# Optimization experiments

Measured on AMD Instinct MI355X. Metric: run time of the kernel, lower is better.

Reference implementation:

```python
import jax, jax.numpy as jnp
import numpy as np

KW = 3          # kernel_width
PAD = (KW - 1) // 2


def setup_inputs() -> dict:
    key = jax.random.key(0)
    ks = jax.random.split(key, 7)
    B, Lq, Lk, D, C = 8, 1024, 1024, 512, 512  # D=q_size, C=k_size
    return {
        "q": jax.random.normal(ks[0], (B, Lq, D), jnp.float32),
        "k": jax.random.normal(ks[1], (B, Lk, C), jnp.float32),
        "W_kernel": jax.random.normal(ks[2], (D, C * KW), jnp.float32) * (1.0 / np.sqrt(D)),
        "b_kernel": jax.random.normal(ks[3], (C * KW,), jnp.float32) * 0.02,
        "W_bias": jax.random.normal(ks[4], (D, 1), jnp.float32) * (1.0 / np.sqrt(D)),
        "b_bias": jax.random.normal(ks[5], (1,), jnp.float32) * 0.02,
        "bias_b": jax.random.normal(ks[6], (1,), jnp.float32),
    }


def reference(q, k, W_kernel, b_kernel, W_bias, b_bias, bias_b):
    B, Lq, D = q.shape
    _, Lk, C = k.shape
    # per-(batch, query) dynamic conv kernels: [B, Lq, C, KW]
    kernel = (q @ W_kernel + b_kernel).reshape(B, Lq, C, KW)
    # per-(batch, query) scalar bias: [B, Lq]
    bias = (q @ W_bias + b_bias)[..., 0]
    # windowed view of k (cross-correlation with 'same' padding)
    kpad = jnp.pad(k, ((0, 0), (PAD, PAD), (0, 0)))  # [B, Lk+2*PAD, C]
    win_idx = jnp.arange(Lk)[:, None] + jnp.arange(KW)[None, :]  # [Lk, KW]
    kwin = kpad[:, win_idx, :]  # [B, Lk, KW, C]
    # a[b,i,j] = sum_{c,w} kernel[b,i,c,w] * kpad[b, j+w, c] + bias[b,i] + bias_b
    a_ij = jnp.einsum('bicw,bjwc->bij', kernel, kwin)
    return a_ij + bias[:, :, None] + bias_b
```

## Files before the change

kernel.cpp:

```cpp
#include <hip/hip_runtime.h>


typedef __attribute__((ext_vector_type(8))) short s8vec;
typedef __attribute__((ext_vector_type(4))) float floatx4;

__device__ __forceinline__ unsigned short f2bf(float f) {
    union { float f; unsigned u; } v; v.f = f;
    unsigned r = (v.u + 0x7FFFu + ((v.u >> 16) & 1u)) >> 16;
    return (unsigned short)r;
}

__device__ __forceinline__ float bf2f(unsigned short s) {
    union { unsigned u; float f; } v; v.u = ((unsigned)s) << 16;
    return v.f;
}

__device__ __forceinline__ void gl2lds16(const void* g, void* l) {
    __builtin_amdgcn_global_load_lds(
        (__attribute__((address_space(1))) void*)(g),
        (__attribute__((address_space(3))) void*)(l), 16, 0, 0);
}

__global__ void cvt_all(const float* __restrict__ q, const float* __restrict__ k,
                        unsigned short* __restrict__ qbf, unsigned short* __restrict__ kp,
                        const float* __restrict__ W, unsigned short* __restrict__ Wt2,
                        const float* __restrict__ b_kernel) {
    int blk = blockIdx.x;
    if (blk < 4104) {
        int t = blk * 256 + threadIdx.x;
        if (t < 524288) {
            const float4* p = (const float4*)q + 2 * (size_t)t;
            float4 a = p[0], b = p[1];
            union { unsigned short s[8]; uint4 v; } o;
            o.s[0]=f2bf(a.x); o.s[1]=f2bf(a.y); o.s[2]=f2bf(a.z); o.s[3]=f2bf(a.w);
            o.s[4]=f2bf(b.x); o.s[5]=f2bf(b.y); o.s[6]=f2bf(b.z); o.s[7]=f2bf(b.w);
            ((uint4*)qbf)[t] = o.v;
        } else if (t < 1048576) {
            int e8 = t - 524288;
            size_t e = (size_t)e8 * 8;
            int b = e8 >> 16;
            int j = (e8 >> 6) & 1023;
            int c = (e8 & 63) * 8;
            const float4* p = (const float4*)(k + e);
            float4 a = p[0], bb = p[1];
            union { unsigned short s[8]; uint4 v; } o;
            o.s[0]=f2bf(a.x); o.s[1]=f2bf(a.y); o.s[2]=f2bf(a.z); o.s[3]=f2bf(a.w);
            o.s[4]=f2bf(bb.x); o.s[5]=f2bf(bb.y); o.s[6]=f2bf(bb.z); o.s[7]=f2bf(bb.w);
            *(uint4*)(kp + ((size_t)(b * 1028 + j + 1) * 512 + c)) = o.v;
        } else if (t < 1050624) {
            int z = t - 1048576;
            int b = z >> 8, r = (z >> 6) & 3, ch = z & 63;
            int row = r ? (1024 + r) : 0;
            *(uint4*)(kp + ((size_t)(b * 1028 + row) * 512 + ch * 8)) = make_uint4(0u,0u,0u,0u);
        }
    } else if (blk < 4616) {
        __shared__ float ldsw[1536];
        int d = blk - 4104;
        const float4* wrow = (const float4*)(W + (size_t)d * 1536);
        for (int e = threadIdx.x; e < 384; e += 256) {
            float4 v = wrow[e];
            float va[4] = { v.x, v.y, v.z, v.w };
            #pragma unroll
            for (int i = 0; i < 4; i++) {
                int idx = e * 4 + i;
                int c = idx / 3, w = idx - c * 3;
                ldsw[w * 512 + c] = va[i];
            }
        }
        __syncthreads();
        for (int p = threadIdx.x; p < 192; p += 256) {
            union { unsigned short s[8]; uint4 v; } o;
            #pragma unroll
            for (int i = 0; i < 8; i++) o.s[i] = f2bf(ldsw[p * 8 + i]);
            *(uint4*)(Wt2 + (size_t)d * 1536 + p * 8) = o.v;
        }
    } else {
        int u = (blk - 4616) * 256 + threadIdx.x;
        int row = 512 + u / 192;
        int p = u - (u / 192) * 192;
        union { unsigned short s[8]; uint4 v; } o;
        if (row == 512) {
            #pragma unroll
            for (int i = 0; i < 8; i++) {
                int lin = p * 8 + i;
                int w = lin >> 9, c = lin & 511;
                o.s[i] = f2bf(b_kernel[c * 3 + w]);
            }
        } else {
            o.v = make_uint4(0u, 0u, 0u, 0u);
        }
        *(uint4*)(Wt2 + (size_t)row * 1536 + p * 8) = o.v;
    }
}

__global__ __launch_bounds__(256) void gemm_V(const unsigned short* __restrict__ kp,
                                              const unsigned short* __restrict__ Wt2,
                                              const float* __restrict__ Wbias,
                                              unsigned short* __restrict__ V) {
    __shared__ unsigned short lds_a[2][128 * 32];
    __shared__ unsigned short lds_b[2][64 * 32];
    int g = blockIdx.x;
    int b = g & 7, slot = g >> 3;
    int j0 = (slot / 9) * 128;
    int n0 = (slot % 9) * 64;
    int tid = threadIdx.x, wid = tid >> 6, lane = tid & 63;
    int wm = wid >> 1, wn = wid & 1;
    int arow = lane >> 2, acol = (lane & 3) * 8;
    const unsigned short* kpb = kp + (size_t)(b * 1028 + j0) * 512;
    floatx4 acc[4][2] = {};

    auto STAGE = [&](int buf, int kk) {
        #pragma unroll
        for (int s = 0; s < 3; ++s) {
            int t = wid * 3 + s;
            if (t < 8) {
                const unsigned short* ga = kpb + (size_t)(t * 16 + arow) * 512 + kk + acol;
                gl2lds16(ga, (char*)lds_a[buf] + t * 1024);
            } else {
                int u = t - 8;
                const unsigned short* gb = Wt2 + (size_t)(n0 + u * 16 + arow) * 1536 + kk + acol;
                gl2lds16(gb, (char*)lds_b[buf] + u * 1024);
            }
        }
    };

    STAGE(0, 0);
    __syncthreads();
    int cur = 0;
    int ra = lane & 15, q8 = (lane >> 4) * 8;
    for (int kt = 0; kt < 48; ++kt) {
        if (kt < 47) STAGE(cur ^ 1, (kt + 1) * 32);
        s8vec af[4], bfr[2];
        #pragma unroll
        for (int mi = 0; mi < 4; mi++)
            af[mi] = *(const s8vec*)(&lds_a[cur][(wm * 64 + mi * 16 + ra) * 32 + q8]);
        #pragma unroll
        for (int ni = 0; ni < 2; ni++)
            bfr[ni] = *(const s8vec*)(&lds_b[cur][(wn * 32 + ni * 16 + ra) * 32 + q8]);
        #pragma unroll
        for (int mi = 0; mi < 4; mi++)
            #pragma unroll
            for (int ni = 0; ni < 2; ni++)
                acc[mi][ni] = __builtin_amdgcn_mfma_f32_16x16x32_bf16(af[mi], bfr[ni], acc[mi][ni], 0, 0, 0);
        if (kt < 47) { __syncthreads(); cur ^= 1; }
    }

    int cl = lane & 15, qd = lane >> 4;
    #pragma unroll
    for (int mi = 0; mi < 4; mi++) {
        #pragma unroll
        for (int ni = 0; ni < 2; ni++) {
            int col = n0 + wn * 32 + ni * 16 + cl;
            float wb = (col < 512) ? Wbias[col] : 0.0f;
            #pragma unroll
            for (int r = 0; r < 4; r++) {
                int m_g = b * 1024 + j0 + wm * 64 + mi * 16 + qd * 4 + r;
                V[(size_t)m_g * 576 + col] = f2bf(acc[mi][ni][r] + wb);
            }
        }
    }
}

__global__ __launch_bounds__(256) void gemm_QV(const unsigned short* __restrict__ qbf,
                                               const unsigned short* __restrict__ V,
                                               const float* __restrict__ b_bias,
                                               const float* __restrict__ bias_b,
                                               float* __restrict__ out) {
    __shared__ unsigned short lds_a[2][128 * 32];
    __shared__ unsigned short lds_b[2][128 * 32];
    int g = blockIdx.x;
    int b = g & 7, slot = g >> 3;
    int i0 = (slot >> 3) * 128;
    int j0 = (slot & 7) * 128;
    int tid = threadIdx.x, wid = tid >> 6, lane = tid & 63;
    int wm = wid >> 1, wn = wid & 1;
    int arow = lane >> 2, acol = (lane & 3) * 8;
    const unsigned short* Ab = qbf + (size_t)b * 1024 * 512;
    const unsigned short* Bb = V + (size_t)b * 1024 * 576;
    floatx4 acc[4][4] = {};

    auto STAGE = [&](int buf, int kk) {
        #pragma unroll
        for (int s = 0; s < 2; ++s) {
            int t = wid * 2 + s;
            const unsigned short* ga = Ab + (size_t)(i0 + t * 16 + arow) * 512 + kk + acol;
            gl2lds16(ga, (char*)lds_a[buf] + t * 1024);
            const unsigned short* gb = Bb + (size_t)(j0 + t * 16 + arow) * 576 + kk + acol;
            gl2lds16(gb, (char*)lds_b[buf] + t * 1024);
        }
    };

    STAGE(0, 0);
    __syncthreads();
    int cur = 0;
    int ra = lane & 15, q8 = (lane >> 4) * 8;
    for (int kt = 0; kt < 16; ++kt) {
        if (kt < 15) STAGE(cur ^ 1, (kt + 1) * 32);
        s8vec af[4], bfr[4];
        #pragma unroll
        for (int mi = 0; mi < 4; mi++)
            af[mi] = *(const s8vec*)(&lds_a[cur][(wm * 64 + mi * 16 + ra) * 32 + q8]);
        #pragma unroll
        for (int ni = 0; ni < 4; ni++)
            bfr[ni] = *(const s8vec*)(&lds_b[cur][(wn * 64 + ni * 16 + ra) * 32 + q8]);
        #pragma unroll
        for (int mi = 0; mi < 4; mi++)
            #pragma unroll
            for (int ni = 0; ni < 4; ni++)
                acc[mi][ni] = __builtin_amdgcn_mfma_f32_16x16x32_bf16(af[mi], bfr[ni], acc[mi][ni], 0, 0, 0);
        if (kt < 15) { __syncthreads(); cur ^= 1; }
    }

    int cl = lane & 15, qd = lane >> 4;
    float bbsum = b_bias[0] + bias_b[0];
    float tv[4];
    #pragma unroll
    for (int ni = 0; ni < 4; ni++) {
        int j_loc = wn * 64 + ni * 16 + cl;
        tv[ni] = bf2f(V[((size_t)(b * 1024 + j0 + j_loc)) * 576 + 512]) + bbsum;
    }
    #pragma unroll
    for (int mi = 0; mi < 4; mi++) {
        #pragma unroll
        for (int r = 0; r < 4; r++) {
            int i_g = i0 + wm * 64 + mi * 16 + qd * 4 + r;
            float* orow = out + ((size_t)(b * 1024 + i_g)) * 1024 + j0;
            #pragma unroll
            for (int ni = 0; ni < 4; ni++) {
                int j_loc = wn * 64 + ni * 16 + cl;
                orow[j_loc] = acc[mi][ni][r] + tv[ni];
            }
        }
    }
}

extern "C" void kernel_launch(void* const* d_in, const int* in_sizes, int n_in,
                              void* d_out, int out_size, void* d_ws, size_t ws_size,
                              hipStream_t stream) {
    const float* q        = (const float*)d_in[0];
    const float* k        = (const float*)d_in[1];
    const float* W_kernel = (const float*)d_in[2];
    const float* b_kernel = (const float*)d_in[3];
    const float* W_bias   = (const float*)d_in[4];
    const float* b_bias   = (const float*)d_in[5];
    const float* bias_b   = (const float*)d_in[6];
    float* out = (float*)d_out;

    char* ws = (char*)d_ws;
    unsigned short* q_bf = (unsigned short*)(ws);
    unsigned short* kp   = (unsigned short*)(ws + 8388608);
    unsigned short* Wt2  = (unsigned short*)(ws + 8388608 + 8421376 + 16384);
    unsigned short* V    = (unsigned short*)(ws + 8388608 + 8421376 + 16384 + 1769472);

    cvt_all<<<4664, 256, 0, stream>>>(q, k, q_bf, kp, W_kernel, Wt2, b_kernel);
    gemm_V<<<576, 256, 0, stream>>>(kp, Wt2, W_bias, V);
    gemm_QV<<<512, 256, 0, stream>>>(q_bf, V, b_bias, bias_b, out);
}
```

Measured before the change: 138.3 us.

## Compute b_kernel bias term separately, shrink V width, use K=64 tiles with XOR swizzle

Moves the b_kernel·kwin bias term out of the augmented GEMM into a separate fp32 reduction in the conversion kernel, so V becomes 512 wide instead of 576 and gemm_V needs 512 blocks instead of 576. Both GEMMs now stage 64-wide K tiles with an XOR-swizzled LDS layout, which halves the number of barriers and is meant to reduce LDS bank conflicts. The cost is double the LDS per block, which may lower occupancy, plus an extra 256-block reduction pass over k.

```diff
diff --git a/kernel.cpp b/kernel.cpp
--- a/kernel.cpp
+++ b/kernel.cpp
@@ -10,11 +10,6 @@
     return (unsigned short)r;
 }
 
-__device__ __forceinline__ float bf2f(unsigned short s) {
-    union { unsigned u; float f; } v; v.u = ((unsigned)s) << 16;
-    return v.f;
-}
-
 __device__ __forceinline__ void gl2lds16(const void* g, void* l) {
     __builtin_amdgcn_global_load_lds(
         (__attribute__((address_space(1))) void*)(g),
@@ -24,7 +19,8 @@
 __global__ void cvt_all(const float* __restrict__ q, const float* __restrict__ k,
                         unsigned short* __restrict__ qbf, unsigned short* __restrict__ kp,
                         const float* __restrict__ W, unsigned short* __restrict__ Wt2,
-                        const float* __restrict__ b_kernel) {
+                        const float* __restrict__ b_kernel, float* __restrict__ tj) {
+    __shared__ float ldsw[1536];
     int blk = blockIdx.x;
     if (blk < 4104) {
         int t = blk * 256 + threadIdx.x;
@@ -54,7 +50,6 @@
             *(uint4*)(kp + ((size_t)(b * 1028 + row) * 512 + ch * 8)) = make_uint4(0u,0u,0u,0u);
         }
     } else if (blk < 4616) {
-        __shared__ float ldsw[1536];
         int d = blk - 4104;
         const float4* wrow = (const float4*)(W + (size_t)d * 1536);
         for (int e = threadIdx.x; e < 384; e += 256) {
@@ -75,21 +70,39 @@
             *(uint4*)(Wt2 + (size_t)d * 1536 + p * 8) = o.v;
         }
     } else {
-        int u = (blk - 4616) * 256 + threadIdx.x;
-        int row = 512 + u / 192;
-        int p = u - (u / 192) * 192;
-        union { unsigned short s[8]; uint4 v; } o;
-        if (row == 512) {
-            #pragma unroll
-            for (int i = 0; i < 8; i++) {
-                int lin = p * 8 + i;
-                int w = lin >> 9, c = lin & 511;
-                o.s[i] = f2bf(b_kernel[c * 3 + w]);
-            }
-        } else {
-            o.v = make_uint4(0u, 0u, 0u, 0u);
-        }
-        *(uint4*)(Wt2 + (size_t)row * 1536 + p * 8) = o.v;
+        int p = blk - 4616;
+        int b = p >> 5, j0r = (p & 31) * 32;
+        for (int e = threadIdx.x; e < 1536; e += 256) {
+            float v = b_kernel[e];
+            int c = e / 3, w = e - c * 3;
+            ldsw[w * 512 + c] = v;
+        }
+        __syncthreads();
+        int wave = threadIdx.x >> 6, lane = threadIdx.x & 63;
+        float bw[3][8];
+        #pragma unroll
+        for (int w = 0; w < 3; w++)
+            #pragma unroll
+            for (int i = 0; i < 8; i++) bw[w][i] = ldsw[w * 512 + lane * 8 + i];
+        const float* kb = k + (size_t)b * 1024 * 512;
+        #pragma unroll
+        for (int rr = 0; rr < 8; rr++) {
+            int j = j0r + wave * 8 + rr;
+            float s = 0.0f;
+            #pragma unroll
+            for (int w = 0; w < 3; w++) {
+                int src = j + w - 1;
+                if (src >= 0 && src < 1024) {
+                    const float4* kr = (const float4*)(kb + (size_t)src * 512) + lane * 2;
+                    float4 a0 = kr[0], a1 = kr[1];
+                    s += a0.x*bw[w][0] + a0.y*bw[w][1] + a0.z*bw[w][2] + a0.w*bw[w][3]
+                       + a1.x*bw[w][4] + a1.y*bw[w][5] + a1.z*bw[w][6] + a1.w*bw[w][7];
+                }
+            }
+            #pragma unroll
+            for (int off = 32; off > 0; off >>= 1) s += __shfl_down(s, off);
+            if (lane == 0) tj[b * 1024 + j] = s;
+        }
     }
 }
 
@@ -97,28 +110,29 @@
                                               const unsigned short* __restrict__ Wt2,
                                               const float* __restrict__ Wbias,
                                               unsigned short* __restrict__ V) {
-    __shared__ unsigned short lds_a[2][128 * 32];
-    __shared__ unsigned short lds_b[2][64 * 32];
+    __shared__ unsigned short lds_a[2][128 * 64];
+    __shared__ unsigned short lds_b[2][64 * 64];
     int g = blockIdx.x;
     int b = g & 7, slot = g >> 3;
-    int j0 = (slot / 9) * 128;
-    int n0 = (slot % 9) * 64;
+    int j0 = (slot >> 3) * 128;
+    int n0 = (slot & 7) * 64;
     int tid = threadIdx.x, wid = tid >> 6, lane = tid & 63;
     int wm = wid >> 1, wn = wid & 1;
-    int arow = lane >> 2, acol = (lane & 3) * 8;
+    int crow = lane >> 3;
+    int scol = ((lane & 7) ^ crow) * 8;
     const unsigned short* kpb = kp + (size_t)(b * 1028 + j0) * 512;
     floatx4 acc[4][2] = {};
 
     auto STAGE = [&](int buf, int kk) {
         #pragma unroll
-        for (int s = 0; s < 3; ++s) {
-            int t = wid * 3 + s;
-            if (t < 8) {
-                const unsigned short* ga = kpb + (size_t)(t * 16 + arow) * 512 + kk + acol;
+        for (int s = 0; s < 6; ++s) {
+            int t = wid * 6 + s;
+            if (t < 16) {
+                const unsigned short* ga = kpb + (size_t)(t * 8 + crow) * 512 + kk + scol;
                 gl2lds16(ga, (char*)lds_a[buf] + t * 1024);
             } else {
-                int u = t - 8;
-                const unsigned short* gb = Wt2 + (size_t)(n0 + u * 16 + arow) * 1536 + kk + acol;
+                int u = t - 16;
+                const unsigned short* gb = Wt2 + (size_t)(n0 + u * 8 + crow) * 1536 + kk + scol;
                 gl2lds16(gb, (char*)lds_b[buf] + u * 1024);
             }
         }
@@ -127,22 +141,29 @@
     STAGE(0, 0);
     __syncthreads();
     int cur = 0;
-    int ra = lane & 15, q8 = (lane >> 4) * 8;
-    for (int kt = 0; kt < 48; ++kt) {
-        if (kt < 47) STAGE(cur ^ 1, (kt + 1) * 32);
-        s8vec af[4], bfr[2];
-        #pragma unroll
-        for (int mi = 0; mi < 4; mi++)
-            af[mi] = *(const s8vec*)(&lds_a[cur][(wm * 64 + mi * 16 + ra) * 32 + q8]);
-        #pragma unroll
-        for (int ni = 0; ni < 2; ni++)
-            bfr[ni] = *(const s8vec*)(&lds_b[cur][(wn * 32 + ni * 16 + ra) * 32 + q8]);
-        #pragma unroll
-        for (int mi = 0; mi < 4; mi++)
-            #pragma unroll
-            for (int ni = 0; ni < 2; ni++)
-                acc[mi][ni] = __builtin_amdgcn_mfma_f32_16x16x32_bf16(af[mi], bfr[ni], acc[mi][ni], 0, 0, 0);
-        if (kt < 47) { __syncthreads(); cur ^= 1; }
+    int ra = lane & 15, hi = lane >> 4;
+    for (int kt = 0; kt < 24; ++kt) {
+        if (kt < 23) STAGE(cur ^ 1, (kt + 1) * 64);
+        #pragma unroll
+        for (int ks = 0; ks < 2; ++ks) {
+            s8vec af[4], bfr[2];
+            #pragma unroll
+            for (int mi = 0; mi < 4; mi++) {
+                int R = wm * 64 + mi * 16 + ra;
+                af[mi] = *(const s8vec*)((const char*)lds_a[cur] + R * 128 + (((ks << 2) + hi) ^ (R & 7)) * 16);
+            }
+            #pragma unroll
+            for (int ni = 0; ni < 2; ni++) {
+                int R = wn * 32 + ni * 16 + ra;
+                bfr[ni] = *(const s8vec*)((const char*)lds_b[cur] + R * 128 + (((ks << 2) + hi) ^ (R & 7)) * 16);
+            }
+            #pragma unroll
+            for (int mi = 0; mi < 4; mi++)
+                #pragma unroll
+                for (int ni = 0; ni < 2; ni++)
+                    acc[mi][ni] = __builtin_amdgcn_mfma_f32_16x16x32_bf16(af[mi], bfr[ni], acc[mi][ni], 0, 0, 0);
+        }
+        if (kt < 23) { __syncthreads(); cur ^= 1; }
     }
 
     int cl = lane & 15, qd = lane >> 4;
@@ -151,11 +172,11 @@
         #pragma unroll
         for (int ni = 0; ni < 2; ni++) {
             int col = n0 + wn * 32 + ni * 16 + cl;
-            float wb = (col < 512) ? Wbias[col] : 0.0f;
+            float wb = Wbias[col];
             #pragma unroll
             for (int r = 0; r < 4; r++) {
                 int m_g = b * 1024 + j0 + wm * 64 + mi * 16 + qd * 4 + r;
-                V[(size_t)m_g * 576 + col] = f2bf(acc[mi][ni][r] + wb);
+                V[(size_t)m_g * 512 + col] = f2bf(acc[mi][ni][r] + wb);
             }
         }
     }
@@ -163,52 +184,65 @@
 
 __global__ __launch_bounds__(256) void gemm_QV(const unsigned short* __restrict__ qbf,
                                                const unsigned short* __restrict__ V,
+                                               const float* __restrict__ tj,
                                                const float* __restrict__ b_bias,
                                                const float* __restrict__ bias_b,
                                                float* __restrict__ out) {
-    __shared__ unsigned short lds_a[2][128 * 32];
-    __shared__ unsigned short lds_b[2][128 * 32];
+    __shared__ unsigned short lds_a[2][128 * 64];
+    __shared__ unsigned short lds_b[2][128 * 64];
     int g = blockIdx.x;
     int b = g & 7, slot = g >> 3;
     int i0 = (slot >> 3) * 128;
     int j0 = (slot & 7) * 128;
     int tid = threadIdx.x, wid = tid >> 6, lane = tid & 63;
     int wm = wid >> 1, wn = wid & 1;
-    int arow = lane >> 2, acol = (lane & 3) * 8;
+    int crow = lane >> 3;
+    int scol = ((lane & 7) ^ crow) * 8;
     const unsigned short* Ab = qbf + (size_t)b * 1024 * 512;
-    const unsigned short* Bb = V + (size_t)b * 1024 * 576;
+    const unsigned short* Bb = V + (size_t)b * 1024 * 512;
     floatx4 acc[4][4] = {};
 
     auto STAGE = [&](int buf, int kk) {
         #pragma unroll
-        for (int s = 0; s < 2; ++s) {
-            int t = wid * 2 + s;
-            const unsigned short* ga = Ab + (size_t)(i0 + t * 16 + arow) * 512 + kk + acol;
-            gl2lds16(ga, (char*)lds_a[buf] + t * 1024);
-            const unsigned short* gb = Bb + (size_t)(j0 + t * 16 + arow) * 576 + kk + acol;
-            gl2lds16(gb, (char*)lds_b[buf] + t * 1024);
+        for (int s = 0; s < 8; ++s) {
+            int t = wid * 8 + s;
+            if (t < 16) {
+                const unsigned short* ga = Ab + (size_t)(i0 + t * 8 + crow) * 512 + kk + scol;
+                gl2lds16(ga, (char*)lds_a[buf] + t * 1024);
+            } else {
+                int u = t - 16;
+                const unsigned short* gb = Bb + (size_t)(j0 + u * 8 + crow) * 512 + kk + scol;
+                gl2lds16(gb, (char*)lds_b[buf] + u * 1024);
+            }
         }
     };
 
     STAGE(0, 0);
     __syncthreads();
     int cur = 0;
-    int ra = lane & 15, q8 = (lane >> 4) * 8;
-    for (int kt = 0; kt < 16; ++kt) {
-        if (kt < 15) STAGE(cur ^ 1, (kt + 1) * 32);
-        s8vec af[4], bfr[4];
-        #pragma unroll
-        for (int mi = 0; mi < 4; mi++)
-            af[mi] = *(const s8vec*)(&lds_a[cur][(wm * 64 + mi * 16 + ra) * 32 + q8]);
-        #pragma unroll
-        for (int ni = 0; ni < 4; ni++)
-            bfr[ni] = *(const s8vec*)(&lds_b[cur][(wn * 64 + ni * 16 + ra) * 32 + q8]);
-        #pragma unroll
-        for (int mi = 0; mi < 4; mi++)
-            #pragma unroll
-            for (int ni = 0; ni < 4; ni++)
-                acc[mi][ni] = __builtin_amdgcn_mfma_f32_16x16x32_bf16(af[mi], bfr[ni], acc[mi][ni], 0, 0, 0);
-        if (kt < 15) { __syncthreads(); cur ^= 1; }
+    int ra = lane & 15, hi = lane >> 4;
+    for (int kt = 0; kt < 8; ++kt) {
+        if (kt < 7) STAGE(cur ^ 1, (kt + 1) * 64);
+        #pragma unroll
+        for (int ks = 0; ks < 2; ++ks) {
+            s8vec af[4], bfr[4];
+            #pragma unroll
+            for (int mi = 0; mi < 4; mi++) {
+                int R = wm * 64 + mi * 16 + ra;
+                af[mi] = *(const s8vec*)((const char*)lds_a[cur] + R * 128 + (((ks << 2) + hi) ^ (R & 7)) * 16);
+            }
+            #pragma unroll
+            for (int ni = 0; ni < 4; ni++) {
+                int R = wn * 64 + ni * 16 + ra;
+                bfr[ni] = *(const s8vec*)((const char*)lds_b[cur] + R * 128 + (((ks << 2) + hi) ^ (R & 7)) * 16);
+            }
+            #pragma unroll
+            for (int mi = 0; mi < 4; mi++)
+                #pragma unroll
+                for (int ni = 0; ni < 4; ni++)
+                    acc[mi][ni] = __builtin_amdgcn_mfma_f32_16x16x32_bf16(af[mi], bfr[ni], acc[mi][ni], 0, 0, 0);
+        }
+        if (kt < 7) { __syncthreads(); cur ^= 1; }
     }
 
     int cl = lane & 15, qd = lane >> 4;
@@ -217,7 +251,7 @@
     #pragma unroll
     for (int ni = 0; ni < 4; ni++) {
         int j_loc = wn * 64 + ni * 16 + cl;
-        tv[ni] = bf2f(V[((size_t)(b * 1024 + j0 + j_loc)) * 576 + 512]) + bbsum;
+        tv[ni] = tj[b * 1024 + j0 + j_loc] + bbsum;
     }
     #pragma unroll
     for (int mi = 0; mi < 4; mi++) {
@@ -250,9 +284,10 @@
     unsigned short* q_bf = (unsigned short*)(ws);
     unsigned short* kp   = (unsigned short*)(ws + 8388608);
     unsigned short* Wt2  = (unsigned short*)(ws + 8388608 + 8421376 + 16384);
-    unsigned short* V    = (unsigned short*)(ws + 8388608 + 8421376 + 16384 + 1769472);
-
-    cvt_all<<<4664, 256, 0, stream>>>(q, k, q_bf, kp, W_kernel, Wt2, b_kernel);
-    gemm_V<<<576, 256, 0, stream>>>(kp, Wt2, W_bias, V);
-    gemm_QV<<<512, 256, 0, stream>>>(q_bf, V, b_bias, bias_b, out);
-}
+    unsigned short* V    = (unsigned short*)(ws + 8388608 + 8421376 + 16384 + 1572864);
+    float*          tj   = (float*)(ws + 8388608 + 8421376 + 16384 + 1572864 + 8388608);
+
+    cvt_all<<<4872, 256, 0, stream>>>(q, k, q_bf, kp, W_kernel, Wt2, b_kernel, tj);
+    gemm_V<<<512, 256, 0, stream>>>(kp, Wt2, W_bias, V);
+    gemm_QV<<<512, 256, 0, stream>>>(q_bf, V, tj, b_bias, bias_b, out);
+}
```

Result: faster. 133.4 us (-3.5%).
